# Optimization experiments

Hardware: AMD Instinct MI355X
Metric: run time of the kernel (lower is better)

## Reference

```python
import jax, jax.numpy as jnp
import numpy as np

B, S, DD, DE, DA = 32, 2048, 1024, 1024, 1024
NEG = -1000000000.0


def setup_inputs() -> dict:
    key = jax.random.key(0)
    k1, k2, k3, k4, k5 = jax.random.split(key, 5)
    query_state = jax.random.normal(k1, (B, DD), dtype=jnp.float32)
    encoder_hidden_states = jax.random.normal(k2, (B, S, DE), dtype=jnp.float32)
    attention_mask = jax.random.randint(k3, (B, S), 0, 2, dtype=jnp.int32)
    # W_c: Linear(DD+DE -> DA, bias=False): weight shape [DA, DD+DE]
    W_c = jax.random.normal(k4, (DA, DD + DE), dtype=jnp.float32) / np.sqrt(DD + DE)
    # V: Linear(DA -> 1, bias=False): weight shape [1, DA]
    V = jax.random.normal(k5, (1, DA), dtype=jnp.float32) / np.sqrt(DA)
    return {
        "query_state": query_state,
        "encoder_hidden_states": encoder_hidden_states,
        "attention_mask": attention_mask,
        "W_c": W_c,
        "V": V,
    }


def reference(query_state, encoder_hidden_states, attention_mask, W_c, V):
    # Split W_c along input dim: cat([q, e]) @ W_c.T == q @ Wq.T + e @ We.T
    Wq = W_c[:, :DD]          # [DA, DD]
    We = W_c[:, DD:]          # [DA, DE]
    q_proj = jnp.einsum('bd,ad->ba', query_state, Wq)            # [B, DA]
    e_proj = jnp.einsum('bsd,ad->bsa', encoder_hidden_states, We)  # [B, S, DA]
    energies = jnp.tanh(q_proj[:, None, :] + e_proj)             # [B, S, DA]
    scores = jnp.einsum('bsa,a->bs', energies, V[0])             # [B, S]
    scores = jnp.where(attention_mask == 0, NEG, scores)
    attention_weights = jax.nn.softmax(scores, axis=1)           # [B, S]
    context_vector = jnp.einsum('bs,bsd->bd', attention_weights, encoder_hidden_states)
    return context_vector, attention_weights
```

## Files before the change

### kernel.cpp

```cpp
#include <hip/hip_runtime.h>
#include <hip/hip_bf16.h>

#define NB 32
#define NS 2048
#define NDD 1024
#define NDE 1024
#define NDA 1024
#define NEGV (-1000000000.0f)

typedef __attribute__((ext_vector_type(8))) __bf16 bf16x8;
typedef __attribute__((ext_vector_type(4))) float f32x4;

__device__ __forceinline__ float fast_tanh(float x) {
    x = fminf(10.0f, fmaxf(-10.0f, x));
    float e = __expf(2.0f * x);
    return __fdividef(e - 1.0f, e + 1.0f);
}

__device__ __forceinline__ float bfu2f(unsigned short v) {
    union { unsigned u; float f; } c; c.u = (unsigned)v << 16; return c.f;
}

__global__ void prep_we(const float* __restrict__ Wc, __bf16* __restrict__ We) {
    int f = blockIdx.x * 256 + threadIdx.x;
    int a  = f >> 8;
    int k4 = f & 255;
    float4 v = *reinterpret_cast<const float4*>(Wc + (size_t)a * (NDD + NDE) + NDD + k4 * 4);
    union { __bf16 h[4]; uint2 u; } pk;
    pk.h[0] = (__bf16)v.x; pk.h[1] = (__bf16)v.y;
    pk.h[2] = (__bf16)v.z; pk.h[3] = (__bf16)v.w;
    *reinterpret_cast<uint2*>(We + (size_t)a * NDE + k4 * 4) = pk.u;
}

__global__ void prep_e(const float* __restrict__ E, __bf16* __restrict__ Eb) {
    size_t i = ((size_t)blockIdx.x * 256 + threadIdx.x) * 8;
    f32x4 x = __builtin_nontemporal_load(reinterpret_cast<const f32x4*>(E + i));
    f32x4 y = __builtin_nontemporal_load(reinterpret_cast<const f32x4*>(E + i + 4));
    union { __bf16 h[8]; uint4 u; } pk;
    pk.h[0] = (__bf16)x[0]; pk.h[1] = (__bf16)x[1]; pk.h[2] = (__bf16)x[2]; pk.h[3] = (__bf16)x[3];
    pk.h[4] = (__bf16)y[0]; pk.h[5] = (__bf16)y[1]; pk.h[6] = (__bf16)y[2]; pk.h[7] = (__bf16)y[3];
    *reinterpret_cast<uint4*>(Eb + i) = pk.u;
}

__global__ void qproj_kernel(const float* __restrict__ q, const float* __restrict__ Wc,
                             float* __restrict__ qp) {
    __shared__ float qs[NDD];
    int b = blockIdx.y;
    int a = blockIdx.x * 256 + threadIdx.x;
    float4 qv = *reinterpret_cast<const float4*>(q + (size_t)b * NDD + threadIdx.x * 4);
    *reinterpret_cast<float4*>(qs + threadIdx.x * 4) = qv;
    __syncthreads();
    const float* wrow = Wc + (size_t)a * (NDD + NDE);
    float acc = 0.f;
#pragma unroll 4
    for (int k4 = 0; k4 < 256; ++k4) {
        float4 w = *reinterpret_cast<const float4*>(wrow + k4 * 4);
        acc += qs[k4*4+0] * w.x + qs[k4*4+1] * w.y + qs[k4*4+2] * w.z + qs[k4*4+3] * w.w;
    }
    qp[(size_t)b * NDA + a] = acc;
}

__global__ __launch_bounds__(1024, 2) void score256(
    const __bf16* __restrict__ Eb, const __bf16* __restrict__ We,
    const float* __restrict__ qp, const float* __restrict__ Vv,
    float* __restrict__ sp) {
    __shared__ __align__(16) __bf16 As[2][256 * 32];
    __shared__ __align__(16) __bf16 Bs[2][256 * 32];

    const int tid  = threadIdx.x;
    const int lane = tid & 63;
    const int l15  = lane & 15;
    const int h    = lane >> 4;
    const int wid  = tid >> 6;
    const int wr   = wid >> 2;
    const int wc   = wid & 3;

    const int bid = blockIdx.x;
    const int xcd = bid & 7;
    const int j   = bid >> 3;
    const int m   = xcd * 32 + (j >> 2);
    const int n   = j & 3;
    const int row0  = m * 256;
    const int ncol0 = n * 256;
    const int b     = m >> 3;

    f32x4 acc[4][4];
#pragma unroll
    for (int mf = 0; mf < 4; ++mf)
#pragma unroll
        for (int nf = 0; nf < 4; ++nf)
            acc[mf][nf] = (f32x4){0.f, 0.f, 0.f, 0.f};

    const int r_st  = tid >> 2;
    const int sg_st = (tid & 3) ^ ((r_st >> 1) & 3);
    const int offE  = (row0  + r_st) * 1024 + sg_st * 8;
    const int offW  = (ncol0 + r_st) * 1024 + sg_st * 8;

    int aoff[4], boff[4];
#pragma unroll
    for (int mf = 0; mf < 4; ++mf) {
        int r = wr * 64 + mf * 16 + l15;
        aoff[mf] = r * 64 + ((h ^ ((r >> 1) & 3)) << 4);
    }
#pragma unroll
    for (int nf = 0; nf < 4; ++nf) {
        int r = wc * 64 + nf * 16 + l15;
        boff[nf] = r * 64 + ((h ^ ((r >> 1) & 3)) << 4);
    }

#define STAGE(buf, kc)                                                                  \
    {                                                                                   \
        __builtin_amdgcn_global_load_lds(                                               \
            (const __attribute__((address_space(1))) unsigned*)(Eb + offE + (kc)),      \
            (__attribute__((address_space(3))) unsigned*)((char*)&As[buf][0] + wid * 1024), \
            16, 0, 0);                                                                  \
        __builtin_amdgcn_global_load_lds(                                               \
            (const __attribute__((address_space(1))) unsigned*)(We + offW + (kc)),      \
            (__attribute__((address_space(3))) unsigned*)((char*)&Bs[buf][0] + wid * 1024), \
            16, 0, 0);                                                                  \
    }

    STAGE(0, 0)
    float qv[4], vv[4];
#pragma unroll
    for (int nf = 0; nf < 4; ++nf) {
        int col = ncol0 + wc * 64 + nf * 16 + l15;
        qv[nf] = qp[(size_t)b * NDA + col];
        vv[nf] = Vv[col];
    }
    __syncthreads();

    for (int T = 0; T < 32; ++T) {
        const int cur = T & 1;
        const char* Ab = (const char*)&As[cur][0];
        const char* Bb = (const char*)&Bs[cur][0];
        if (T < 31) STAGE(cur ^ 1, (T + 1) * 32)

        bf16x8 afr[4], bfr[4];
#pragma unroll
        for (int nf = 0; nf < 4; ++nf)
            bfr[nf] = *reinterpret_cast<const bf16x8*>(Bb + boff[nf]);
#pragma unroll
        for (int mf = 0; mf < 4; ++mf)
            afr[mf] = *reinterpret_cast<const bf16x8*>(Ab + aoff[mf]);
        __builtin_amdgcn_s_setprio(1);
#pragma unroll
        for (int mf = 0; mf < 4; ++mf)
#pragma unroll
            for (int nf = 0; nf < 4; ++nf)
                acc[mf][nf] = __builtin_amdgcn_mfma_f32_16x16x32_bf16(afr[mf], bfr[nf], acc[mf][nf], 0, 0, 0);
        __builtin_amdgcn_s_setprio(0);
        __syncthreads();
    }

    float* ps2 = reinterpret_cast<float*>(&As[0][0]);
#pragma unroll
    for (int mf = 0; mf < 4; ++mf)
#pragma unroll
        for (int jj = 0; jj < 4; ++jj) {
            float s = 0.f;
#pragma unroll
            for (int nf = 0; nf < 4; ++nf)
                s += fast_tanh(qv[nf] + acc[mf][nf][jj]) * vv[nf];
            s += __shfl_xor(s, 1);
            s += __shfl_xor(s, 2);
            s += __shfl_xor(s, 4);
            s += __shfl_xor(s, 8);
            if (l15 == 0)
                ps2[(wr * 64 + mf * 16 + h * 4 + jj) * 4 + wc] = s;
        }
    __syncthreads();
    if (tid < 256)
        sp[(size_t)n * (NB * NS) + row0 + tid] =
            ps2[tid * 4] + ps2[tid * 4 + 1] + ps2[tid * 4 + 2] + ps2[tid * 4 + 3];
}

__global__ void softmax_kernel(const float* __restrict__ sp, const int* __restrict__ mask,
                               float* __restrict__ wout, int np) {
    int b = blockIdx.x;
    const int* mrow = mask + (size_t)b * NS;
    float v[8];
    float lmax = -INFINITY;
#pragma unroll
    for (int jj = 0; jj < 8; ++jj) {
        int s = threadIdx.x + 256 * jj;
        float sc = 0.f;
        for (int nn = 0; nn < np; ++nn) sc += sp[(size_t)nn * (NB * NS) + b * NS + s];
        v[jj] = (mrow[s] == 0) ? NEGV : sc;
        lmax = fmaxf(lmax, v[jj]);
    }
#pragma unroll
    for (int mm = 1; mm <= 32; mm <<= 1) lmax = fmaxf(lmax, __shfl_xor(lmax, mm));
    __shared__ float redm[4], reds[4];
    if ((threadIdx.x & 63) == 0) redm[threadIdx.x >> 6] = lmax;
    __syncthreads();
    float bmax = fmaxf(fmaxf(redm[0], redm[1]), fmaxf(redm[2], redm[3]));
    float lsum = 0.f;
#pragma unroll
    for (int jj = 0; jj < 8; ++jj) { v[jj] = __expf(v[jj] - bmax); lsum += v[jj]; }
#pragma unroll
    for (int mm = 1; mm <= 32; mm <<= 1) lsum += __shfl_xor(lsum, mm);
    if ((threadIdx.x & 63) == 0) reds[threadIdx.x >> 6] = lsum;
    __syncthreads();
    float inv = __fdividef(1.0f, reds[0] + reds[1] + reds[2] + reds[3]);
#pragma unroll
    for (int jj = 0; jj < 8; ++jj) wout[(size_t)b * NS + threadIdx.x + 256 * jj] = v[jj] * inv;
}

__global__ void context_bf16(const __bf16* __restrict__ Eb, const float* __restrict__ w,
                             float* __restrict__ ctx) {
    int b  = blockIdx.x >> 3;
    int dc = blockIdx.x & 7;
    int dg = threadIdx.x & 31;
    int ss = threadIdx.x >> 5;
    const __bf16* base = Eb + (size_t)b * NS * NDE + (size_t)(ss * 256) * NDE + dc * 128 + dg * 4;
    const float* wb = w + (size_t)b * NS + ss * 256;
    float a0 = 0.f, a1 = 0.f, a2 = 0.f, a3 = 0.f;
#pragma unroll 8
    for (int s = 0; s < 256; ++s) {
        float ws = wb[s];
        uint2 u = *reinterpret_cast<const uint2*>(base + (size_t)s * NDE);
        a0 = fmaf(ws, bfu2f((unsigned short)(u.x & 0xffff)), a0);
        a1 = fmaf(ws, bfu2f((unsigned short)(u.x >> 16)), a1);
        a2 = fmaf(ws, bfu2f((unsigned short)(u.y & 0xffff)), a2);
        a3 = fmaf(ws, bfu2f((unsigned short)(u.y >> 16)), a3);
    }
    __shared__ float4 part[256];
    part[threadIdx.x] = make_float4(a0, a1, a2, a3);
    __syncthreads();
    if (threadIdx.x < 32) {
        float4 r = part[threadIdx.x];
#pragma unroll
        for (int k = 1; k < 8; ++k) {
            float4 p = part[threadIdx.x + 32 * k];
            r.x += p.x; r.y += p.y; r.z += p.z; r.w += p.w;
        }
        *reinterpret_cast<float4*>(ctx + (size_t)b * NDD + dc * 128 + threadIdx.x * 4) = r;
    }
}

extern "C" void kernel_launch(void* const* d_in, const int* in_sizes, int n_in,
                              void* d_out, int out_size, void* d_ws, size_t ws_size,
                              hipStream_t stream) {
    const float* query = (const float*)d_in[0];
    const float* enc   = (const float*)d_in[1];
    const int*   mask  = (const int*)d_in[2];
    const float* Wc    = (const float*)d_in[3];
    const float* V     = (const float*)d_in[4];

    float* out = (float*)d_out;
    float* ctx = out;
    float* wts = out + NB * NDD;

    const size_t WE_B = (size_t)NDA * NDE * 2;
    const size_t QP_B = (size_t)NB * NDA * 4;
    const size_t SP_B = (size_t)8 * NB * NS * 4;
    char* ws = (char*)d_ws;
    __bf16* We = (__bf16*)ws;
    float*  qp = (float*)(ws + WE_B);
    float*  sp = (float*)(ws + WE_B + QP_B);
    __bf16* Eb = (__bf16*)(ws + WE_B + QP_B + SP_B);

    hipLaunchKernelGGL(prep_we,      dim3(1024),  dim3(256), 0, stream, Wc, We);
    hipLaunchKernelGGL(qproj_kernel, dim3(4, NB), dim3(256), 0, stream, query, Wc, qp);
    hipLaunchKernelGGL(prep_e,       dim3(32768), dim3(256), 0, stream, enc, Eb);
    hipLaunchKernelGGL(score256,     dim3(1024),  dim3(1024), 0, stream, Eb, We, qp, V, sp);
    hipLaunchKernelGGL(softmax_kernel, dim3(NB),  dim3(256), 0, stream, sp, mask, wts, 4);
    hipLaunchKernelGGL(context_bf16, dim3(256),   dim3(256), 0, stream, Eb, wts, ctx);
}
```

Before: 295.3 us.

## Enlarge score GEMM tile to 512 rows to halve weight reloads

The score kernel now computes 512 encoder rows per block instead of 256, doubling the M-tile and per-thread accumulators. Each block stages two E chunks per k-step, and the grid shrinks to 512 blocks. The aim is to reuse each loaded We tile across twice as many rows, cutting global and LDS traffic for the weight operand. The costs are a larger LDS footprint, 128 accumulator registers per thread, and a tightened launch bound (1024, 4) that can force register spills and lower occupancy.

```diff
diff --git a/kernel.cpp b/kernel.cpp
--- a/kernel.cpp
+++ b/kernel.cpp
@@ -60,11 +60,11 @@
     qp[(size_t)b * NDA + a] = acc;
 }
 
-__global__ __launch_bounds__(1024, 2) void score256(
+__global__ __launch_bounds__(1024, 4) void score256(
     const __bf16* __restrict__ Eb, const __bf16* __restrict__ We,
     const float* __restrict__ qp, const float* __restrict__ Vv,
     float* __restrict__ sp) {
-    __shared__ __align__(16) __bf16 As[2][256 * 32];
+    __shared__ __align__(16) __bf16 As[2][512 * 32];
     __shared__ __align__(16) __bf16 Bs[2][256 * 32];
 
     const int tid  = threadIdx.x;
@@ -78,28 +78,35 @@
     const int bid = blockIdx.x;
     const int xcd = bid & 7;
     const int j   = bid >> 3;
-    const int m   = xcd * 32 + (j >> 2);
+    const int m   = xcd * 16 + (j >> 2);
     const int n   = j & 3;
-    const int row0  = m * 256;
+    const int row0  = m * 512;
     const int ncol0 = n * 256;
-    const int b     = m >> 3;
-
-    f32x4 acc[4][4];
-#pragma unroll
-    for (int mf = 0; mf < 4; ++mf)
+    const int b     = m >> 2;
+
+    f32x4 acc[8][4];
+#pragma unroll
+    for (int mf = 0; mf < 8; ++mf)
 #pragma unroll
         for (int nf = 0; nf < 4; ++nf)
             acc[mf][nf] = (f32x4){0.f, 0.f, 0.f, 0.f};
 
-    const int r_st  = tid >> 2;
-    const int sg_st = (tid & 3) ^ ((r_st >> 1) & 3);
-    const int offE  = (row0  + r_st) * 1024 + sg_st * 8;
-    const int offW  = (ncol0 + r_st) * 1024 + sg_st * 8;
-
-    int aoff[4], boff[4];
-#pragma unroll
-    for (int mf = 0; mf < 4; ++mf) {
-        int r = wr * 64 + mf * 16 + l15;
+    int offE[2];
+#pragma unroll
+    for (int i = 0; i < 2; ++i) {
+        int chunk = i * 1024 + tid;
+        int r  = chunk >> 2;
+        int sg = (chunk & 3) ^ ((r >> 1) & 3);
+        offE[i] = (row0 + r) * 1024 + sg * 8;
+    }
+    const int r_stw  = tid >> 2;
+    const int sg_stw = (tid & 3) ^ ((r_stw >> 1) & 3);
+    const int offW   = (ncol0 + r_stw) * 1024 + sg_stw * 8;
+
+    int aoff[8], boff[4];
+#pragma unroll
+    for (int mf = 0; mf < 8; ++mf) {
+        int r = wr * 128 + mf * 16 + l15;
         aoff[mf] = r * 64 + ((h ^ ((r >> 1) & 3)) << 4);
     }
 #pragma unroll
@@ -110,10 +117,12 @@
 
 #define STAGE(buf, kc)                                                                  \
     {                                                                                   \
-        __builtin_amdgcn_global_load_lds(                                               \
-            (const __attribute__((address_space(1))) unsigned*)(Eb + offE + (kc)),      \
-            (__attribute__((address_space(3))) unsigned*)((char*)&As[buf][0] + wid * 1024), \
-            16, 0, 0);                                                                  \
+        _Pragma("unroll")                                                               \
+        for (int i = 0; i < 2; ++i)                                                     \
+            __builtin_amdgcn_global_load_lds(                                           \
+                (const __attribute__((address_space(1))) unsigned*)(Eb + offE[i] + (kc)),\
+                (__attribute__((address_space(3))) unsigned*)((char*)&As[buf][0] + i * 16384 + wid * 1024), \
+                16, 0, 0);                                                              \
         __builtin_amdgcn_global_load_lds(                                               \
             (const __attribute__((address_space(1))) unsigned*)(We + offW + (kc)),      \
             (__attribute__((address_space(3))) unsigned*)((char*)&Bs[buf][0] + wid * 1024), \
@@ -125,7 +134,7 @@
 #pragma unroll
     for (int nf = 0; nf < 4; ++nf) {
         int col = ncol0 + wc * 64 + nf * 16 + l15;
-        qv[nf] = qp[(size_t)b * NDA + col];
+        qv[nf] = qp[(size_t)(row0 >> 11) * NDA + col];
         vv[nf] = Vv[col];
     }
     __syncthreads();
@@ -136,26 +145,34 @@
         const char* Bb = (const char*)&Bs[cur][0];
         if (T < 31) STAGE(cur ^ 1, (T + 1) * 32)
 
-        bf16x8 afr[4], bfr[4];
+        bf16x8 bfr[4];
 #pragma unroll
         for (int nf = 0; nf < 4; ++nf)
             bfr[nf] = *reinterpret_cast<const bf16x8*>(Bb + boff[nf]);
 #pragma unroll
-        for (int mf = 0; mf < 4; ++mf)
-            afr[mf] = *reinterpret_cast<const bf16x8*>(Ab + aoff[mf]);
-        __builtin_amdgcn_s_setprio(1);
-#pragma unroll
-        for (int mf = 0; mf < 4; ++mf)
+        for (int mf = 0; mf < 4; ++mf) {
+            bf16x8 a0 = *reinterpret_cast<const bf16x8*>(Ab + aoff[mf]);
+            __builtin_amdgcn_s_setprio(1);
 #pragma unroll
             for (int nf = 0; nf < 4; ++nf)
-                acc[mf][nf] = __builtin_amdgcn_mfma_f32_16x16x32_bf16(afr[mf], bfr[nf], acc[mf][nf], 0, 0, 0);
-        __builtin_amdgcn_s_setprio(0);
+                acc[mf][nf] = __builtin_amdgcn_mfma_f32_16x16x32_bf16(a0, bfr[nf], acc[mf][nf], 0, 0, 0);
+            __builtin_amdgcn_s_setprio(0);
+        }
+#pragma unroll
+        for (int mf = 4; mf < 8; ++mf) {
+            bf16x8 a0 = *reinterpret_cast<const bf16x8*>(Ab + aoff[mf]);
+            __builtin_amdgcn_s_setprio(1);
+#pragma unroll
+            for (int nf = 0; nf < 4; ++nf)
+                acc[mf][nf] = __builtin_amdgcn_mfma_f32_16x16x32_bf16(a0, bfr[nf], acc[mf][nf], 0, 0, 0);
+            __builtin_amdgcn_s_setprio(0);
+        }
         __syncthreads();
     }
 
     float* ps2 = reinterpret_cast<float*>(&As[0][0]);
 #pragma unroll
-    for (int mf = 0; mf < 4; ++mf)
+    for (int mf = 0; mf < 8; ++mf)
 #pragma unroll
         for (int jj = 0; jj < 4; ++jj) {
             float s = 0.f;
@@ -167,12 +184,13 @@
             s += __shfl_xor(s, 4);
             s += __shfl_xor(s, 8);
             if (l15 == 0)
-                ps2[(wr * 64 + mf * 16 + h * 4 + jj) * 4 + wc] = s;
-        }
-    __syncthreads();
-    if (tid < 256)
+                ps2[(wr * 128 + mf * 16 + h * 4 + jj) * 4 + wc] = s;
+        }
+    __syncthreads();
+    if (tid < 512)
         sp[(size_t)n * (NB * NS) + row0 + tid] =
             ps2[tid * 4] + ps2[tid * 4 + 1] + ps2[tid * 4 + 2] + ps2[tid * 4 + 3];
+    (void)b;
 }
 
 __global__ void softmax_kernel(const float* __restrict__ sp, const int* __restrict__ mask,
@@ -264,7 +282,7 @@
     hipLaunchKernelGGL(prep_we,      dim3(1024),  dim3(256), 0, stream, Wc, We);
     hipLaunchKernelGGL(qproj_kernel, dim3(4, NB), dim3(256), 0, stream, query, Wc, qp);
     hipLaunchKernelGGL(prep_e,       dim3(32768), dim3(256), 0, stream, enc, Eb);
-    hipLaunchKernelGGL(score256,     dim3(1024),  dim3(1024), 0, stream, Eb, We, qp, V, sp);
+    hipLaunchKernelGGL(score256,     dim3(512),   dim3(1024), 0, stream, Eb, We, qp, V, sp);
     hipLaunchKernelGGL(softmax_kernel, dim3(NB),  dim3(256), 0, stream, sp, mask, wts, 4);
     hipLaunchKernelGGL(context_bf16, dim3(256),   dim3(256), 0, stream, Eb, wts, ctx);
 }
```

Result: slower. 893.5 us (+202.6%).
